# Performance work log

Hardware: AMD Instinct MI355X
Metric: run time of the kernel (lower is better)

Reference implementation:

```python
import jax, jax.numpy as jnp
import numpy as np

N = 100000      # nodes
E = 1000000     # edges
G = 1024        # graphs
NODE_IN, CLIMBER_IN, HID, OUT, HEADS = 6, 4, 64, 4, 2
SLOPE = 0.2     # PyG GATConv default negative_slope


def gat_conv(x, edge_index, W, att_src, att_dst, bias):
    """PyG GATConv, heads=HEADS, concat=False (mean over heads), add_self_loops=True."""
    heads, ch = att_src.shape
    xp = (x @ W).reshape(-1, heads, ch)                       # [N,H,C]
    a_src = jnp.einsum('nhc,hc->nh', xp, att_src)             # [N,H]
    a_dst = jnp.einsum('nhc,hc->nh', xp, att_dst)
    loops = jnp.arange(x.shape[0])
    src = jnp.concatenate([edge_index[0], loops])             # [E+N]
    dst = jnp.concatenate([edge_index[1], loops])
    e = jax.nn.leaky_relu(a_src[src] + a_dst[dst], SLOPE)     # [E+N,H]
    emax = jax.ops.segment_max(e, dst, num_segments=x.shape[0])
    emax = jnp.where(jnp.isfinite(emax), emax, 0.0)
    ex = jnp.exp(e - emax[dst])
    den = jax.ops.segment_sum(ex, dst, num_segments=x.shape[0])
    alpha = ex / (den[dst] + 1e-16)                           # segment softmax over incoming edges
    msg = xp[src] * alpha[:, :, None]                         # [E+N,H,C]
    agg = jax.ops.segment_sum(msg, dst, num_segments=x.shape[0])  # [N,H,C]
    return agg.mean(axis=1) + bias                            # concat=False -> head mean


def setup_inputs() -> dict:
    key = jax.random.key(0)
    ks = jax.random.split(key, 20)
    s = lambda *d: 1.0 / np.sqrt(d[0])
    inp = {
        'x': jax.random.normal(ks[0], (N, NODE_IN), jnp.float32),
        'edge_index': jax.random.randint(ks[1], (2, E), 0, N),
        'batch': jnp.sort(jax.random.randint(ks[2], (N,), 0, G)),
        'climber': jax.random.normal(ks[3], (G, CLIMBER_IN), jnp.float32),
        # conv1 params
        'W1': jax.random.normal(ks[4], (NODE_IN, HEADS * HID), jnp.float32) * s(NODE_IN),
        'as1': jax.random.normal(ks[5], (HEADS, HID), jnp.float32) * s(HID),
        'ad1': jax.random.normal(ks[6], (HEADS, HID), jnp.float32) * s(HID),
        'b1': jnp.zeros((HID,), jnp.float32),
        # conv2 params
        'W2': jax.random.normal(ks[7], (HID, HEADS * HID), jnp.float32) * s(HID),
        'as2': jax.random.normal(ks[8], (HEADS, HID), jnp.float32) * s(HID),
        'ad2': jax.random.normal(ks[9], (HEADS, HID), jnp.float32) * s(HID),
        'b2': jnp.zeros((HID,), jnp.float32),
        # climber embed
        'Wc': jax.random.normal(ks[10], (CLIMBER_IN, HID), jnp.float32) * s(CLIMBER_IN),
        'bc': jnp.zeros((HID,), jnp.float32),
        # classifier
        'Wm1': jax.random.normal(ks[11], (2 * HID, HID), jnp.float32) * s(2 * HID),
        'bm1': jnp.zeros((HID,), jnp.float32),
        'Wm2': jax.random.normal(ks[12], (HID, OUT), jnp.float32) * s(HID),
        'bm2': jnp.zeros((OUT,), jnp.float32),
    }
    return inp


def reference(x, edge_index, batch, climber, W1, as1, ad1, b1, W2, as2, ad2, b2,
              Wc, bc, Wm1, bm1, Wm2, bm2):
    h = jax.nn.relu(gat_conv(x, edge_index, W1, as1, ad1, b1))
    h = jax.nn.relu(gat_conv(h, edge_index, W2, as2, ad2, b2))
    c = jax.nn.relu(climber @ Wc + bc)            # dropout is identity in eval mode
    z = jnp.concatenate([h, c[batch]], axis=1)    # [N, 2*HID]
    z = jax.nn.relu(z @ Wm1 + bm1)                # dropout identity (eval)
    return z @ Wm2 + bm2                          # [N, OUT]
```

## Files before the change

kernel.cpp:

```cpp
#include <hip/hip_runtime.h>
#include <hip/hip_fp16.h>

#define SLOPE 0.2f

__device__ __forceinline__ float lrelu(float v) { return v >= 0.f ? v : SLOPE * v; }

__device__ __forceinline__ unsigned pack2(float a, float b) {
    __half2 h = __floats2half2_rn(a, b);
    return *reinterpret_cast<unsigned*>(&h);
}
__device__ __forceinline__ float4 h4tof4(uint2 u) {
    __half2 a = *reinterpret_cast<__half2*>(&u.x);
    __half2 b = *reinterpret_cast<__half2*>(&u.y);
    float2 fa = __half22float2(a), fb = __half22float2(b);
    return make_float4(fa.x, fa.y, fb.x, fb.y);
}
__device__ __forceinline__ void acc8(float4& A, float4& B, float a, uint4 u) {
    float4 lo = h4tof4(make_uint2(u.x, u.y));
    float4 hi = h4tof4(make_uint2(u.z, u.w));
    A.x += a * lo.x; A.y += a * lo.y; A.z += a * lo.z; A.w += a * lo.w;
    B.x += a * hi.x; B.y += a * hi.y; B.z += a * hi.z; B.w += a * hi.w;
}

template <int K>
__global__ __launch_bounds__(256)
void k_xp_gemm(const float* __restrict__ x, const float* __restrict__ W,
               const float* __restrict__ as_, const float* __restrict__ ad_,
               __half* __restrict__ xph, float* __restrict__ asrc,
               float* __restrict__ adst, int N) {
    constexpr int ZS = K + 1;
    __shared__ float zs[64 * ZS];
    __shared__ float ws[K * 128];
    const int n0 = blockIdx.x * 64;
    const int t = threadIdx.x;

    for (int i = t; i < K * 32; i += 256) ((float4*)ws)[i] = ((const float4*)W)[i];
    for (int i = t; i < 64 * K; i += 256) {
        int n = i / K, k = i - n * K;
        int gn = n0 + n;
        zs[n * ZS + k] = (gn < N) ? x[(size_t)gn * K + k] : 0.f;
    }
    __syncthreads();

    const int tx = t & 15, ty = t >> 4;
    const int c0a = tx * 4;
    const int c0b = 64 + tx * 4;

    float4 asA = *(const float4*)(as_ + c0a);
    float4 asB = *(const float4*)(as_ + c0b);
    float4 adA = *(const float4*)(ad_ + c0a);
    float4 adB = *(const float4*)(ad_ + c0b);

    float acc[4][8];
    #pragma unroll
    for (int i = 0; i < 4; ++i)
        #pragma unroll
        for (int j = 0; j < 8; ++j) acc[i][j] = 0.f;

    for (int k = 0; k < K; ++k) {
        float4 w0 = *(const float4*)(ws + k * 128 + c0a);
        float4 w1 = *(const float4*)(ws + k * 128 + c0b);
        #pragma unroll
        for (int i = 0; i < 4; ++i) {
            float zv = zs[(ty * 4 + i) * ZS + k];
            acc[i][0] += zv * w0.x; acc[i][1] += zv * w0.y;
            acc[i][2] += zv * w0.z; acc[i][3] += zv * w0.w;
            acc[i][4] += zv * w1.x; acc[i][5] += zv * w1.y;
            acc[i][6] += zv * w1.z; acc[i][7] += zv * w1.w;
        }
    }

    #pragma unroll
    for (int i = 0; i < 4; ++i) {
        int nl = ty * 4 + i, gn = n0 + nl;
        if (gn < N) {
            uint2 ua, ub;
            ua.x = pack2(acc[i][0], acc[i][1]);
            ua.y = pack2(acc[i][2], acc[i][3]);
            ub.x = pack2(acc[i][4], acc[i][5]);
            ub.y = pack2(acc[i][6], acc[i][7]);
            *(uint2*)(xph + (size_t)gn * 128 + c0a) = ua;
            *(uint2*)(xph + (size_t)gn * 128 + c0b) = ub;
        }
        float ps0 = acc[i][0]*asA.x + acc[i][1]*asA.y + acc[i][2]*asA.z + acc[i][3]*asA.w;
        float ps1 = acc[i][4]*asB.x + acc[i][5]*asB.y + acc[i][6]*asB.z + acc[i][7]*asB.w;
        float pd0 = acc[i][0]*adA.x + acc[i][1]*adA.y + acc[i][2]*adA.z + acc[i][3]*adA.w;
        float pd1 = acc[i][4]*adB.x + acc[i][5]*adB.y + acc[i][6]*adB.z + acc[i][7]*adB.w;
        #pragma unroll
        for (int off = 1; off <= 8; off <<= 1) {
            ps0 += __shfl_xor(ps0, off, 64);
            ps1 += __shfl_xor(ps1, off, 64);
            pd0 += __shfl_xor(pd0, off, 64);
            pd1 += __shfl_xor(pd1, off, 64);
        }
        if (tx == 0 && gn < N) {
            asrc[gn * 2]     = ps0;
            asrc[gn * 2 + 1] = ps1;
            adst[gn * 2]     = pd0;
            adst[gn * 2 + 1] = pd1;
        }
    }
}

__global__ void k_hist(const int* __restrict__ dst, int* __restrict__ deg,
                       int* __restrict__ rank, int E) {
    int e = blockIdx.x * blockDim.x + threadIdx.x;
    if (e < E) rank[e] = atomicAdd(&deg[dst[e]], 1);
}

__global__ void k_scan_partial(const int* __restrict__ deg, int* __restrict__ partial, int N) {
    int b = blockIdx.x, t = threadIdx.x;
    int base = b * 1024 + t * 4;
    int s = 0;
    for (int i = 0; i < 4; ++i) { int idx = base + i; if (idx < N) s += deg[idx]; }
    __shared__ int sh[256];
    sh[t] = s; __syncthreads();
    for (int off = 128; off > 0; off >>= 1) { if (t < off) sh[t] += sh[t + off]; __syncthreads(); }
    if (t == 0) partial[b] = sh[0];
}

__global__ void k_scan_final(const int* __restrict__ deg, const int* __restrict__ partial,
                             int* __restrict__ rowptr, int N, int E, int nb) {
    int b = blockIdx.x, t = threadIdx.x;
    __shared__ int shp[256];
    shp[t] = (t < nb) ? partial[t] : 0;
    __syncthreads();
    for (int off = 1; off < 256; off <<= 1) {
        int v = (t >= off) ? shp[t - off] : 0;
        __syncthreads();
        shp[t] += v;
        __syncthreads();
    }
    int pbase = (b > 0) ? shp[b - 1] : 0;
    __syncthreads();

    int base = b * 1024 + t * 4;
    int local[4]; int s = 0;
    for (int i = 0; i < 4; ++i) { int idx = base + i; local[i] = (idx < N) ? deg[idx] : 0; s += local[i]; }
    __shared__ int sh[256];
    int orig = s;
    sh[t] = s; __syncthreads();
    for (int off = 1; off < 256; off <<= 1) {
        int v = (t >= off) ? sh[t - off] : 0;
        __syncthreads();
        sh[t] += v;
        __syncthreads();
    }
    int run = pbase + sh[t] - orig;
    for (int i = 0; i < 4; ++i) {
        int idx = base + i;
        if (idx < N) rowptr[idx] = run;
        run += local[i];
    }
    if (b == 0 && t == 0) rowptr[N] = E;
}

__global__ void k_scatter(const int* __restrict__ src, const int* __restrict__ dst,
                          const int* __restrict__ rowptr, const int* __restrict__ rank,
                          int* __restrict__ csr_src, int E) {
    int e = blockIdx.x * blockDim.x + threadIdx.x;
    if (e >= E) return;
    int d = dst[e];
    csr_src[rowptr[d] + rank[e]] = src[e];
}

__global__ void k_ag(const int* __restrict__ rowptr, const int* __restrict__ csr_src,
                     const float* __restrict__ asrc, const float* __restrict__ adst,
                     const __half* __restrict__ xph, const float* __restrict__ b,
                     float* __restrict__ hout, int N) {
    int tid = blockIdx.x * blockDim.x + threadIdx.x;
    int lane = threadIdx.x & 63;
    int wid = tid >> 6;
    int nw = (gridDim.x * blockDim.x) >> 6;
    const int l  = lane & 31;
    const int hh = lane >> 5;
    const int g8 = (lane >> 3) & 3;
    const int c8 = lane & 7;
    const uint4* xp4 = (const uint4*)xph;
    float4 bb0 = ((const float4*)b)[c8 * 2];
    float4 bb1 = ((const float4*)b)[c8 * 2 + 1];

    for (int n = wid; n < N; n += nw) {
        int rs = rowptr[n], re = rowptr[n + 1], cnt = re - rs;
        float a_dst = adst[n * 2 + hh];
        float eself = __expf(lrelu(asrc[n * 2 + hh] + a_dst));

        float4 accA = make_float4(0.f, 0.f, 0.f, 0.f);
        float4 accB = make_float4(0.f, 0.f, 0.f, 0.f);

        if (cnt <= 32) {
            float ev = 0.f; int s_reg = n;
            if (l < cnt) {
                s_reg = csr_src[rs + l];
                ev = __expf(lrelu(asrc[s_reg * 2 + hh] + a_dst));
            }
            float den = ev + (l == 0 ? eself : 0.f);
            #pragma unroll
            for (int off = 16; off > 0; off >>= 1) den += __shfl_xor(den, off, 64);
            float inv = 1.f / (den + 1e-16f);
            float alpha_l = ev * inv;

            if (g8 == 0) acc8(accA, accB, eself * inv, xp4[(size_t)n * 16 + hh * 8 + c8]);
            int base = (hh << 5) - rs;
            for (int e0 = rs; e0 < re; e0 += 8) {
                int ea = e0 + g8, eb = e0 + 4 + g8;
                bool va = ea < re, vb = eb < re;
                float aa = __shfl(alpha_l, base + ea, 64);
                int   sa = __shfl(s_reg,   base + ea, 64);
                float ab = __shfl(alpha_l, base + eb, 64);
                int   sb = __shfl(s_reg,   base + eb, 64);
                if (!va) { aa = 0.f; sa = n; }
                if (!vb) { ab = 0.f; sb = n; }
                uint4 u1 = xp4[(size_t)sa * 16 + hh * 8 + c8];
                uint4 u2 = xp4[(size_t)sb * 16 + hh * 8 + c8];
                acc8(accA, accB, aa, u1);
                acc8(accA, accB, ab, u2);
            }
        } else {
            float den = (l == 0) ? eself : 0.f;
            for (int e = rs + l; e < re; e += 32)
                den += __expf(lrelu(asrc[csr_src[e] * 2 + hh] + a_dst));
            #pragma unroll
            for (int off = 16; off > 0; off >>= 1) den += __shfl_xor(den, off, 64);
            float inv = 1.f / (den + 1e-16f);
            if (g8 == 0) acc8(accA, accB, eself * inv, xp4[(size_t)n * 16 + hh * 8 + c8]);
            for (int e0 = rs; e0 < re; e0 += 8) {
                int ea = e0 + g8, eb = e0 + 4 + g8;
                bool va = ea < re, vb = eb < re;
                int sa = va ? csr_src[ea] : n;
                int sb = vb ? csr_src[eb] : n;
                float aa = va ? __expf(lrelu(asrc[sa * 2 + hh] + a_dst)) * inv : 0.f;
                float ab = vb ? __expf(lrelu(asrc[sb * 2 + hh] + a_dst)) * inv : 0.f;
                uint4 u1 = xp4[(size_t)sa * 16 + hh * 8 + c8];
                uint4 u2 = xp4[(size_t)sb * 16 + hh * 8 + c8];
                acc8(accA, accB, aa, u1);
                acc8(accA, accB, ab, u2);
            }
        }

        #pragma unroll
        for (int off = 8; off <= 32; off <<= 1) {
            accA.x += __shfl_xor(accA.x, off, 64);
            accA.y += __shfl_xor(accA.y, off, 64);
            accA.z += __shfl_xor(accA.z, off, 64);
            accA.w += __shfl_xor(accA.w, off, 64);
            accB.x += __shfl_xor(accB.x, off, 64);
            accB.y += __shfl_xor(accB.y, off, 64);
            accB.z += __shfl_xor(accB.z, off, 64);
            accB.w += __shfl_xor(accB.w, off, 64);
        }
        if (lane < 8) {
            float4 r0, r1;
            r0.x = fmaxf(accA.x * 0.5f + bb0.x, 0.f);
            r0.y = fmaxf(accA.y * 0.5f + bb0.y, 0.f);
            r0.z = fmaxf(accA.z * 0.5f + bb0.z, 0.f);
            r0.w = fmaxf(accA.w * 0.5f + bb0.w, 0.f);
            r1.x = fmaxf(accB.x * 0.5f + bb1.x, 0.f);
            r1.y = fmaxf(accB.y * 0.5f + bb1.y, 0.f);
            r1.z = fmaxf(accB.z * 0.5f + bb1.z, 0.f);
            r1.w = fmaxf(accB.w * 0.5f + bb1.w, 0.f);
            ((float4*)hout)[(size_t)n * 16 + c8 * 2]     = r0;
            ((float4*)hout)[(size_t)n * 16 + c8 * 2 + 1] = r1;
        }
    }
}

__global__ __launch_bounds__(256)
void k_climber_cpre(const float* __restrict__ climber, const float* __restrict__ Wc,
                    const float* __restrict__ bc, const float* __restrict__ Wm1,
                    const float* __restrict__ bm1, float* __restrict__ cpre, int G) {
    __shared__ float ce[4][64];
    __shared__ float wm1b[64 * 64];
    int t = threadIdx.x;
    for (int i = t; i < 1024; i += 256) ((float4*)wm1b)[i] = ((const float4*)Wm1)[1024 + i];
    int gl = t >> 6, c = t & 63;
    int g = blockIdx.x * 4 + gl;
    float acc = bc[c];
    if (g < G)
        for (int k = 0; k < 4; ++k) acc += climber[g * 4 + k] * Wc[k * 64 + c];
    ce[gl][c] = fmaxf(acc, 0.f);
    __syncthreads();
    float o = bm1[c];
    for (int k = 0; k < 64; ++k) o += ce[gl][k] * wm1b[k * 64 + c];
    if (g < G) cpre[(size_t)g * 64 + c] = o;
}

__global__ __launch_bounds__(256)
void k_final(const float* __restrict__ h2, const float* __restrict__ cpre,
             const int* __restrict__ batch, const float* __restrict__ Wm1,
             const float* __restrict__ Wm2, const float* __restrict__ bm2,
             float* __restrict__ out, int N) {
    __shared__ float zs[64 * 65];
    __shared__ float ws[64 * 64];
    __shared__ float4 w2l[64];
    const int n0 = blockIdx.x * 64;
    const int t = threadIdx.x;

    for (int i = t; i < 1024; i += 256) ((float4*)ws)[i] = ((const float4*)Wm1)[i];
    if (t < 64) w2l[t] = ((const float4*)Wm2)[t];
    for (int i = t; i < 64 * 64; i += 256) {
        int n = i >> 6, k = i & 63;
        int gn = n0 + n;
        zs[n * 65 + k] = (gn < N) ? h2[(size_t)gn * 64 + k] : 0.f;
    }
    __syncthreads();

    const int tx = t & 15, ty = t >> 4;
    const int c0 = tx * 4;
    float acc[4][4];
    #pragma unroll
    for (int i = 0; i < 4; ++i)
        #pragma unroll
        for (int j = 0; j < 4; ++j) acc[i][j] = 0.f;

    for (int k = 0; k < 64; ++k) {
        float4 wv = *(const float4*)(ws + k * 64 + c0);
        #pragma unroll
        for (int i = 0; i < 4; ++i) {
            float zv = zs[(ty * 4 + i) * 65 + k];
            acc[i][0] += zv * wv.x; acc[i][1] += zv * wv.y;
            acc[i][2] += zv * wv.z; acc[i][3] += zv * wv.w;
        }
    }
    __syncthreads();

    float4 wa = w2l[c0], wb = w2l[c0 + 1], wc = w2l[c0 + 2], wd = w2l[c0 + 3];
    #pragma unroll
    for (int i = 0; i < 4; ++i) {
        int nl = ty * 4 + i, gn = n0 + nl;
        float4 o = make_float4(0.f, 0.f, 0.f, 0.f);
        if (gn < N) {
            int b = batch[gn];
            float4 cp = *(const float4*)(cpre + (size_t)b * 64 + c0);
            float m0 = fmaxf(acc[i][0] + cp.x, 0.f);
            float m1 = fmaxf(acc[i][1] + cp.y, 0.f);
            float m2 = fmaxf(acc[i][2] + cp.z, 0.f);
            float m3 = fmaxf(acc[i][3] + cp.w, 0.f);
            o.x = m0 * wa.x + m1 * wb.x + m2 * wc.x + m3 * wd.x;
            o.y = m0 * wa.y + m1 * wb.y + m2 * wc.y + m3 * wd.y;
            o.z = m0 * wa.z + m1 * wb.z + m2 * wc.z + m3 * wd.z;
            o.w = m0 * wa.w + m1 * wb.w + m2 * wc.w + m3 * wd.w;
        }
        *(float4*)(zs + tx * 260 + nl * 4) = o;
    }
    __syncthreads();
    {
        int nl = t >> 2, j = t & 3, gn = n0 + nl;
        float s = 0.f;
        #pragma unroll
        for (int tx2 = 0; tx2 < 16; ++tx2) s += zs[tx2 * 260 + nl * 4 + j];
        if (gn < N) out[(size_t)gn * 4 + j] = s + bm2[j];
    }
}

extern "C" void kernel_launch(void* const* d_in, const int* in_sizes, int n_in,
                              void* d_out, int out_size, void* d_ws, size_t ws_size,
                              hipStream_t stream) {
    const float* x       = (const float*)d_in[0];
    const int*   ei      = (const int*)  d_in[1];
    const int*   batch   = (const int*)  d_in[2];
    const float* climber = (const float*)d_in[3];
    const float* W1  = (const float*)d_in[4];
    const float* as1 = (const float*)d_in[5];
    const float* ad1 = (const float*)d_in[6];
    const float* b1  = (const float*)d_in[7];
    const float* W2  = (const float*)d_in[8];
    const float* as2 = (const float*)d_in[9];
    const float* ad2 = (const float*)d_in[10];
    const float* b2  = (const float*)d_in[11];
    const float* Wc  = (const float*)d_in[12];
    const float* bc  = (const float*)d_in[13];
    const float* Wm1 = (const float*)d_in[14];
    const float* bm1 = (const float*)d_in[15];
    const float* Wm2 = (const float*)d_in[16];
    const float* bm2 = (const float*)d_in[17];

    const int N  = in_sizes[0] / 6;
    const int E  = in_sizes[1] / 2;
    const int G  = in_sizes[3] / 4;

    const int* srcI = ei;
    const int* dstI = ei + E;

    char* base = (char*)d_ws;
    size_t off = 0;
    auto carve = [&](size_t bytes) { void* p = base + off; off += (bytes + 255) & ~size_t(255); return p; };
    __half* xph   = (__half*)carve((size_t)N * 128 * 2);
    float* hbuf   = (float*)carve((size_t)N * 64 * 4);
    float* asrc   = (float*)carve((size_t)N * 2 * 4);
    float* adst   = (float*)carve((size_t)N * 2 * 4);
    float* cpre   = (float*)carve((size_t)G * 64 * 4);
    int*   deg    = (int*)  carve((size_t)N * 4);
    int*   rowptr = (int*)  carve((size_t)(N + 1) * 4);
    int*   rank   = (int*)  carve((size_t)E * 4);
    int*   partial= (int*)  carve(4096 * 4);
    int*   csr_src= (int*)  carve((size_t)E * 4);

    const int tpb = 256;
    const int nScanBlk = (N + 1023) / 1024;
    const int nEdgeBlk = (E + tpb - 1) / tpb;
    const int PG = 2048;
    const int nTile = (N + 63) / 64;

    hipMemsetAsync(deg, 0, (size_t)N * 4, stream);
    k_hist<<<nEdgeBlk, tpb, 0, stream>>>(dstI, deg, rank, E);
    k_scan_partial<<<nScanBlk, tpb, 0, stream>>>(deg, partial, N);
    k_scan_final<<<nScanBlk, tpb, 0, stream>>>(deg, partial, rowptr, N, E, nScanBlk);
    k_scatter<<<nEdgeBlk, tpb, 0, stream>>>(srcI, dstI, rowptr, rank, csr_src, E);

    k_xp_gemm<6><<<nTile, tpb, 0, stream>>>(x, W1, as1, ad1, xph, asrc, adst, N);
    k_ag<<<PG, tpb, 0, stream>>>(rowptr, csr_src, asrc, adst, xph, b1, hbuf, N);

    k_xp_gemm<64><<<nTile, tpb, 0, stream>>>(hbuf, W2, as2, ad2, xph, asrc, adst, N);
    k_ag<<<PG, tpb, 0, stream>>>(rowptr, csr_src, asrc, adst, xph, b2, hbuf, N);

    k_climber_cpre<<<(G + 3) / 4, tpb, 0, stream>>>(climber, Wc, bc, Wm1, bm1, cpre, G);
    k_final<<<nTile, tpb, 0, stream>>>(hbuf, cpre, batch, Wm1, Wm2, bm2, (float*)d_out, N);
}
```

Before: 341.6 us.

## Fuse second GAT aggregation with classifier MLP into one kernel

```diff
diff --git a/kernel.cpp b/kernel.cpp
--- a/kernel.cpp
+++ b/kernel.cpp
@@ -266,6 +266,143 @@
 }
 
 __global__ __launch_bounds__(256)
+void k_ag_mlp(const int* __restrict__ rowptr, const int* __restrict__ csr_src,
+              const float* __restrict__ asrc, const float* __restrict__ adst,
+              const __half* __restrict__ xph, const float* __restrict__ b,
+              const float* __restrict__ cpre, const int* __restrict__ batch,
+              const float* __restrict__ Wm1, const float* __restrict__ Wm2,
+              const float* __restrict__ bm2, float* __restrict__ out, int N) {
+    __shared__ float wm1a[64 * 64];
+    __shared__ float4 w2l[64];
+    for (int i = threadIdx.x; i < 1024; i += 256) ((float4*)wm1a)[i] = ((const float4*)Wm1)[i];
+    if (threadIdx.x < 64) w2l[threadIdx.x] = ((const float4*)Wm2)[threadIdx.x];
+    __syncthreads();
+
+    int tid = blockIdx.x * blockDim.x + threadIdx.x;
+    int lane = threadIdx.x & 63;
+    int wid = tid >> 6;
+    int nw = (gridDim.x * blockDim.x) >> 6;
+    const int l  = lane & 31;
+    const int hh = lane >> 5;
+    const int g8 = (lane >> 3) & 3;
+    const int c8 = lane & 7;
+    const uint4* xp4 = (const uint4*)xph;
+    float4 bb0 = ((const float4*)b)[c8 * 2];
+    float4 bb1 = ((const float4*)b)[c8 * 2 + 1];
+    float4 w2 = w2l[lane];
+    float4 bm2v = *((const float4*)bm2);
+
+    for (int n = wid; n < N; n += nw) {
+        int rs = rowptr[n], re = rowptr[n + 1], cnt = re - rs;
+        float a_dst = adst[n * 2 + hh];
+        float eself = __expf(lrelu(asrc[n * 2 + hh] + a_dst));
+
+        float4 accA = make_float4(0.f, 0.f, 0.f, 0.f);
+        float4 accB = make_float4(0.f, 0.f, 0.f, 0.f);
+
+        if (cnt <= 32) {
+            float ev = 0.f; int s_reg = n;
+            if (l < cnt) {
+                s_reg = csr_src[rs + l];
+                ev = __expf(lrelu(asrc[s_reg * 2 + hh] + a_dst));
+            }
+            float den = ev + (l == 0 ? eself : 0.f);
+            #pragma unroll
+            for (int off = 16; off > 0; off >>= 1) den += __shfl_xor(den, off, 64);
+            float inv = 1.f / (den + 1e-16f);
+            float alpha_l = ev * inv;
+
+            if (g8 == 0) acc8(accA, accB, eself * inv, xp4[(size_t)n * 16 + hh * 8 + c8]);
+            int base = (hh << 5) - rs;
+            for (int e0 = rs; e0 < re; e0 += 8) {
+                int ea = e0 + g8, eb = e0 + 4 + g8;
+                bool va = ea < re, vb = eb < re;
+                float aa = __shfl(alpha_l, base + ea, 64);
+                int   sa = __shfl(s_reg,   base + ea, 64);
+                float ab = __shfl(alpha_l, base + eb, 64);
+                int   sb = __shfl(s_reg,   base + eb, 64);
+                if (!va) { aa = 0.f; sa = n; }
+                if (!vb) { ab = 0.f; sb = n; }
+                uint4 u1 = xp4[(size_t)sa * 16 + hh * 8 + c8];
+                uint4 u2 = xp4[(size_t)sb * 16 + hh * 8 + c8];
+                acc8(accA, accB, aa, u1);
+                acc8(accA, accB, ab, u2);
+            }
+        } else {
+            float den = (l == 0) ? eself : 0.f;
+            for (int e = rs + l; e < re; e += 32)
+                den += __expf(lrelu(asrc[csr_src[e] * 2 + hh] + a_dst));
+            #pragma unroll
+            for (int off = 16; off > 0; off >>= 1) den += __shfl_xor(den, off, 64);
+            float inv = 1.f / (den + 1e-16f);
+            if (g8 == 0) acc8(accA, accB, eself * inv, xp4[(size_t)n * 16 + hh * 8 + c8]);
+            for (int e0 = rs; e0 < re; e0 += 8) {
+                int ea = e0 + g8, eb = e0 + 4 + g8;
+                bool va = ea < re, vb = eb < re;
+                int sa = va ? csr_src[ea] : n;
+                int sb = vb ? csr_src[eb] : n;
+                float aa = va ? __expf(lrelu(asrc[sa * 2 + hh] + a_dst)) * inv : 0.f;
+                float ab = vb ? __expf(lrelu(asrc[sb * 2 + hh] + a_dst)) * inv : 0.f;
+                uint4 u1 = xp4[(size_t)sa * 16 + hh * 8 + c8];
+                uint4 u2 = xp4[(size_t)sb * 16 + hh * 8 + c8];
+                acc8(accA, accB, aa, u1);
+                acc8(accA, accB, ab, u2);
+            }
+        }
+
+        #pragma unroll
+        for (int off = 8; off <= 32; off <<= 1) {
+            accA.x += __shfl_xor(accA.x, off, 64);
+            accA.y += __shfl_xor(accA.y, off, 64);
+            accA.z += __shfl_xor(accA.z, off, 64);
+            accA.w += __shfl_xor(accA.w, off, 64);
+            accB.x += __shfl_xor(accB.x, off, 64);
+            accB.y += __shfl_xor(accB.y, off, 64);
+            accB.z += __shfl_xor(accB.z, off, 64);
+            accB.w += __shfl_xor(accB.w, off, 64);
+        }
+        float4 r0, r1;
+        r0.x = fmaxf(accA.x * 0.5f + bb0.x, 0.f);
+        r0.y = fmaxf(accA.y * 0.5f + bb0.y, 0.f);
+        r0.z = fmaxf(accA.z * 0.5f + bb0.z, 0.f);
+        r0.w = fmaxf(accA.w * 0.5f + bb0.w, 0.f);
+        r1.x = fmaxf(accB.x * 0.5f + bb1.x, 0.f);
+        r1.y = fmaxf(accB.y * 0.5f + bb1.y, 0.f);
+        r1.z = fmaxf(accB.z * 0.5f + bb1.z, 0.f);
+        r1.w = fmaxf(accB.w * 0.5f + bb1.w, 0.f);
+
+        int bg = batch[n];
+        float m = cpre[(size_t)bg * 64 + lane];
+        #pragma unroll
+        for (int k8 = 0; k8 < 8; ++k8) {
+            float s0 = __shfl(r0.x, k8, 64), s1 = __shfl(r0.y, k8, 64);
+            float s2 = __shfl(r0.z, k8, 64), s3 = __shfl(r0.w, k8, 64);
+            float s4 = __shfl(r1.x, k8, 64), s5 = __shfl(r1.y, k8, 64);
+            float s6 = __shfl(r1.z, k8, 64), s7 = __shfl(r1.w, k8, 64);
+            const float* wr = wm1a + (k8 * 8) * 64 + lane;
+            m += s0 * wr[0]   + s1 * wr[64]  + s2 * wr[128] + s3 * wr[192]
+               + s4 * wr[256] + s5 * wr[320] + s6 * wr[384] + s7 * wr[448];
+        }
+        m = fmaxf(m, 0.f);
+        float4 p;
+        p.x = m * w2.x; p.y = m * w2.y; p.z = m * w2.z; p.w = m * w2.w;
+        #pragma unroll
+        for (int off = 1; off <= 32; off <<= 1) {
+            p.x += __shfl_xor(p.x, off, 64);
+            p.y += __shfl_xor(p.y, off, 64);
+            p.z += __shfl_xor(p.z, off, 64);
+            p.w += __shfl_xor(p.w, off, 64);
+        }
+        if (lane == 0) {
+            float4 o;
+            o.x = p.x + bm2v.x; o.y = p.y + bm2v.y;
+            o.z = p.z + bm2v.z; o.w = p.w + bm2v.w;
+            ((float4*)out)[n] = o;
+        }
+    }
+}
+
+__global__ __launch_bounds__(256)
 void k_climber_cpre(const float* __restrict__ climber, const float* __restrict__ Wc,
                     const float* __restrict__ bc, const float* __restrict__ Wm1,
                     const float* __restrict__ bm1, float* __restrict__ cpre, int G) {
@@ -283,74 +420,6 @@
     float o = bm1[c];
     for (int k = 0; k < 64; ++k) o += ce[gl][k] * wm1b[k * 64 + c];
     if (g < G) cpre[(size_t)g * 64 + c] = o;
-}
-
-__global__ __launch_bounds__(256)
-void k_final(const float* __restrict__ h2, const float* __restrict__ cpre,
-             const int* __restrict__ batch, const float* __restrict__ Wm1,
-             const float* __restrict__ Wm2, const float* __restrict__ bm2,
-             float* __restrict__ out, int N) {
-    __shared__ float zs[64 * 65];
-    __shared__ float ws[64 * 64];
-    __shared__ float4 w2l[64];
-    const int n0 = blockIdx.x * 64;
-    const int t = threadIdx.x;
-
-    for (int i = t; i < 1024; i += 256) ((float4*)ws)[i] = ((const float4*)Wm1)[i];
-    if (t < 64) w2l[t] = ((const float4*)Wm2)[t];
-    for (int i = t; i < 64 * 64; i += 256) {
-        int n = i >> 6, k = i & 63;
-        int gn = n0 + n;
-        zs[n * 65 + k] = (gn < N) ? h2[(size_t)gn * 64 + k] : 0.f;
-    }
-    __syncthreads();
-
-    const int tx = t & 15, ty = t >> 4;
-    const int c0 = tx * 4;
-    float acc[4][4];
-    #pragma unroll
-    for (int i = 0; i < 4; ++i)
-        #pragma unroll
-        for (int j = 0; j < 4; ++j) acc[i][j] = 0.f;
-
-    for (int k = 0; k < 64; ++k) {
-        float4 wv = *(const float4*)(ws + k * 64 + c0);
-        #pragma unroll
-        for (int i = 0; i < 4; ++i) {
-            float zv = zs[(ty * 4 + i) * 65 + k];
-            acc[i][0] += zv * wv.x; acc[i][1] += zv * wv.y;
-            acc[i][2] += zv * wv.z; acc[i][3] += zv * wv.w;
-        }
-    }
-    __syncthreads();
-
-    float4 wa = w2l[c0], wb = w2l[c0 + 1], wc = w2l[c0 + 2], wd = w2l[c0 + 3];
-    #pragma unroll
-    for (int i = 0; i < 4; ++i) {
-        int nl = ty * 4 + i, gn = n0 + nl;
-        float4 o = make_float4(0.f, 0.f, 0.f, 0.f);
-        if (gn < N) {
-            int b = batch[gn];
-            float4 cp = *(const float4*)(cpre + (size_t)b * 64 + c0);
-            float m0 = fmaxf(acc[i][0] + cp.x, 0.f);
-            float m1 = fmaxf(acc[i][1] + cp.y, 0.f);
-            float m2 = fmaxf(acc[i][2] + cp.z, 0.f);
-            float m3 = fmaxf(acc[i][3] + cp.w, 0.f);
-            o.x = m0 * wa.x + m1 * wb.x + m2 * wc.x + m3 * wd.x;
-            o.y = m0 * wa.y + m1 * wb.y + m2 * wc.y + m3 * wd.y;
-            o.z = m0 * wa.z + m1 * wb.z + m2 * wc.z + m3 * wd.z;
-            o.w = m0 * wa.w + m1 * wb.w + m2 * wc.w + m3 * wd.w;
-        }
-        *(float4*)(zs + tx * 260 + nl * 4) = o;
-    }
-    __syncthreads();
-    {
-        int nl = t >> 2, j = t & 3, gn = n0 + nl;
-        float s = 0.f;
-        #pragma unroll
-        for (int tx2 = 0; tx2 < 16; ++tx2) s += zs[tx2 * 260 + nl * 4 + j];
-        if (gn < N) out[(size_t)gn * 4 + j] = s + bm2[j];
-    }
 }
 
 extern "C" void kernel_launch(void* const* d_in, const int* in_sizes, int n_in,
@@ -412,8 +481,7 @@
     k_ag<<<PG, tpb, 0, stream>>>(rowptr, csr_src, asrc, adst, xph, b1, hbuf, N);
 
     k_xp_gemm<64><<<nTile, tpb, 0, stream>>>(hbuf, W2, as2, ad2, xph, asrc, adst, N);
-    k_ag<<<PG, tpb, 0, stream>>>(rowptr, csr_src, asrc, adst, xph, b2, hbuf, N);
-
     k_climber_cpre<<<(G + 3) / 4, tpb, 0, stream>>>(climber, Wc, bc, Wm1, bm1, cpre, G);
-    k_final<<<nTile, tpb, 0, stream>>>(hbuf, cpre, batch, Wm1, Wm2, bm2, (float*)d_out, N);
-}
+    k_ag_mlp<<<PG, tpb, 0, stream>>>(rowptr, csr_src, asrc, adst, xph, b2,
+                                     cpre, batch, Wm1, Wm2, bm2, (float*)d_out, N);
+}
```

Result: slower. 432.8 us (+26.7%).
